# Optimization experiments

Measured on AMD Instinct MI355X. Metric: run time of the kernel, lower is better.

## Reference

```python
import jax, jax.numpy as jnp
import numpy as np

B, N, D = 2, 2048, 1024
H, FD, HD = 16, 16, 64
ENC = 512
EPS = 1e-12
RD = 4.0            # sqrt(scale_dim=feature_dim=16)
RRD = 2.0           # sqrt(RD)
R2 = float(np.sqrt(2.0))


def taylor_exp(x):
    # x: [..., fd] -> [..., 1 + fd + fd*fd]
    x2 = (x[..., :, None] * x[..., None, :]).reshape(*x.shape[:-1], FD * FD) / R2
    return jnp.concatenate([jnp.ones_like(x[..., :1]), x / RRD, x2 / RD], axis=-1)


def setup_inputs() -> dict:
    key = jax.random.key(0)
    ks = jax.random.split(key, 7)
    s = 1.0 / np.sqrt(D)
    x = jax.random.normal(ks[0], (B, N, D), dtype=jnp.float32)
    Wq = jax.random.normal(ks[1], (H * FD, D), dtype=jnp.float32) * s
    Wk = jax.random.normal(ks[2], (H * FD, D), dtype=jnp.float32) * s
    Wv = jax.random.normal(ks[3], (H * HD, D), dtype=jnp.float32) * s
    Wk_enc = jax.random.normal(ks[4], (H * FD, D), dtype=jnp.float32) * s
    Wv_enc = jax.random.normal(ks[5], (H * HD, D), dtype=jnp.float32) * s
    Wout = jax.random.normal(ks[6], (D, H * HD), dtype=jnp.float32) * s
    return {"x": x, "Wq": Wq, "Wk": Wk, "Wv": Wv,
            "Wk_enc": Wk_enc, "Wv_enc": Wv_enc, "Wout": Wout}


def reference(x, Wq, Wk, Wv, Wk_enc, Wv_enc, Wout):
    b, n, _ = x.shape
    # projections -> [b, h, n, *]
    q = (x @ Wq.T).reshape(b, n, H, FD).transpose(0, 2, 1, 3)
    k = (x @ Wk.T).reshape(b, n, H, FD).transpose(0, 2, 1, 3)
    v = (x @ Wv.T).reshape(b, n, H, HD).transpose(0, 2, 1, 3)
    # encoder prefix
    x_enc = x[:, :ENC]
    k_enc = (x_enc @ Wk_enc.T).reshape(b, ENC, H, FD).transpose(0, 2, 1, 3)
    v_enc = (x_enc @ Wv_enc.T).reshape(b, ENC, H, HD).transpose(0, 2, 1, 3)
    # Taylor feature maps: fd -> 1 + fd + fd^2 = 273
    k_enc_f = taylor_exp(k_enc)
    q_f = taylor_exp(q)
    k_f = taylor_exp(k)
    # causal decoder attention (unnormalized)
    A_qk = jnp.einsum('bhnd,bhmd->bhnm', q_f, k_f)
    A_qk = jnp.tril(A_qk)
    y1 = jnp.einsum('bhnm,bhme->bhne', A_qk, v)
    # cross attention to encoder prefix
    A_qk2 = jnp.einsum('bhnd,bhmd->bhnm', q_f, k_enc_f)
    y2 = jnp.einsum('bhnm,bhme->bhne', A_qk2, v_enc)
    # shared normalizer: enc sum + causal cumsum of decoder key features
    k_state = k_enc_f.sum(axis=2, keepdims=True) + jnp.cumsum(k_f, axis=2)
    z = 1.0 / ((q_f * k_state).sum(axis=-1) + EPS)  # [b, h, n]
    out = (y1 + y2) * z[..., None]                  # [b, h, n, hd]
    out = out.transpose(0, 2, 1, 3).reshape(b, n, H * HD)
    return out @ Wout.T
```

## Files before the change

kernel.cpp:

```cpp
#include <hip/hip_runtime.h>

#define B_    2
#define N_    2048
#define H_    16
#define HD_   64
#define ENC_  512
#define FP_   288
#define CHK_  64
#define NC_   32
#define SSZ_  18720
#define C2C_  0.17677669529663687f
#define EPS_  1e-12f

using s8v   = __attribute__((ext_vector_type(8))) short;
using s4v   = __attribute__((ext_vector_type(4))) short;
using h8v   = __attribute__((ext_vector_type(8))) _Float16;
using f4v   = __attribute__((ext_vector_type(4))) float;
using u16x4 = __attribute__((ext_vector_type(4))) unsigned short;
typedef unsigned short ushort_t;

__device__ __forceinline__ unsigned short f16q(float x) {
    _Float16 h = (_Float16)x;
    return __builtin_bit_cast(unsigned short, h);
}
__device__ __forceinline__ float f16f(unsigned short u) {
    return (float)__builtin_bit_cast(_Float16, u);
}
__device__ __forceinline__ u16x4 f16q4(float4 v) {
    return (u16x4){f16q(v.x), f16q(v.y), f16q(v.z), f16q(v.w)};
}

#define MFMAH_ __builtin_amdgcn_mfma_f32_16x16x32_f16

__device__ __forceinline__ void gld16(const void* g, void* l) {
    __builtin_amdgcn_global_load_lds(
        (const __attribute__((address_space(1))) unsigned int*)g,
        (__attribute__((address_space(3))) unsigned int*)l, 16, 0, 0);
}

__device__ __forceinline__ int xcd_swz(int b, int nwg) {
    int q = nwg >> 3, r = nwg & 7;
    int xcd = b & 7, loc = b >> 3;
    return (xcd < r ? xcd * (q + 1) : r * (q + 1) + (xcd - r) * q) + loc;
}

#define X_F4   1048576
#define W1_F4  393216
#define W2_F4  327680
#define WO_F4  262144

__global__ __launch_bounds__(256) void split_all(
    const float* __restrict__ x,
    const float* __restrict__ Wq, const float* __restrict__ Wk,
    const float* __restrict__ Wv, const float* __restrict__ Wke,
    const float* __restrict__ Wve, const float* __restrict__ Wout,
    ushort_t* __restrict__ xh,
    ushort_t* __restrict__ w1, ushort_t* __restrict__ w2,
    ushort_t* __restrict__ wo)
{
    int gid = blockIdx.x * 256 + threadIdx.x;
    if (gid < X_F4) {
        ((u16x4*)xh)[gid] = f16q4(((const float4*)x)[gid]);
    } else if (gid < X_F4 + W1_F4) {
        int i = gid - X_F4;
        int row = i >> 8, c4 = i & 255;
        const float* s = (row < 256) ? Wq + (size_t)row * 1024
                       : (row < 512) ? Wk + (size_t)(row - 256) * 1024
                                     : Wv + (size_t)(row - 512) * 1024;
        ((u16x4*)w1)[i] = f16q4(*(const float4*)(s + c4 * 4));
    } else if (gid < X_F4 + W1_F4 + W2_F4) {
        int i = gid - X_F4 - W1_F4;
        int row = i >> 8, c4 = i & 255;
        const float* s = (row < 256) ? Wke + (size_t)row * 1024
                                     : Wve + (size_t)(row - 256) * 1024;
        ((u16x4*)w2)[i] = f16q4(*(const float4*)(s + c4 * 4));
    } else {
        int i = gid - X_F4 - W1_F4 - W2_F4;
        ((u16x4*)wo)[i] = f16q4(((const float4*)Wout)[i]);
    }
}

template <int SHIFT>
__device__ __forceinline__ void bg128(
    const ushort_t* __restrict__ Ah, const ushort_t* __restrict__ Wh,
    int bx, int by, int rowjump,
    ushort_t* SM, f4v (&acc)[4][4])
{
    int t = threadIdx.x;
    int w = t >> 6, lane = t & 63;
    int row0 = by * 128, col0 = bx * 128;
    int wrow = (w >> 1) * 64, wcol = (w & 1) * 64;
    int fr = lane & 15, g = lane >> 4;

    int c0 = lane, c1 = 64 + lane;
    int r0 = w * 32 + (c0 >> 2), k80 = (c0 & 3) * 8;
    int r1 = w * 32 + (c1 >> 2), k81 = (c1 & 3) * 8;
    int gr0 = row0 + r0, gr1 = row0 + r1;
    size_t a0 = (size_t)(gr0 >> SHIFT) * rowjump + (gr0 & ((1 << SHIFT) - 1));
    size_t a1 = (size_t)(gr1 >> SHIFT) * rowjump + (gr1 & ((1 << SHIFT) - 1));
    const ushort_t* pA0 = Ah + a0 * 1024 + k80;
    const ushort_t* pA1 = Ah + a1 * 1024 + k81;
    const ushort_t* pW0 = Wh + (size_t)(col0 + r0) * 1024 + k80;
    const ushort_t* pW1 = Wh + (size_t)(col0 + r1) * 1024 + k81;
    int woff = w * 1024;

    #pragma unroll
    for (int mt = 0; mt < 4; ++mt)
        #pragma unroll
        for (int nt = 0; nt < 4; ++nt) acc[mt][nt] = (f4v){0.f, 0.f, 0.f, 0.f};

    auto STAGE = [&](int buf, int k0) {
        ushort_t* Bp = SM + buf * 8192;
        gld16(pA0 + k0, Bp + woff);
        gld16(pA1 + k0, Bp + woff + 512);
        gld16(pW0 + k0, Bp + 4096 + woff);
        gld16(pW1 + k0, Bp + 4096 + woff + 512);
    };

    STAGE(0, 0);
    __syncthreads();
    int cur = 0;
    for (int k0 = 0; k0 < 1024; k0 += 32) {
        if (k0 + 32 < 1024) STAGE(cur ^ 1, k0 + 32);
        ushort_t* Bp = SM + cur * 8192;
        h8v a_h[4], b_[4];
        #pragma unroll
        for (int mt = 0; mt < 4; ++mt)
            a_h[mt] = *(const h8v*)&Bp[(wrow + mt * 16 + fr) * 32 + g * 8];
        #pragma unroll
        for (int nt = 0; nt < 4; ++nt)
            b_[nt] = *(const h8v*)&Bp[4096 + (wcol + nt * 16 + fr) * 32 + g * 8];
        #pragma unroll
        for (int mt = 0; mt < 4; ++mt)
            #pragma unroll
            for (int nt = 0; nt < 4; ++nt)
                acc[mt][nt] = MFMAH_(a_h[mt], b_[nt], acc[mt][nt], 0, 0, 0);
        __syncthreads();
        cur ^= 1;
    }
}

__global__ __launch_bounds__(256) void proj2(
    const ushort_t* __restrict__ xh,
    const ushort_t* __restrict__ w1, const ushort_t* __restrict__ w2,
    float* __restrict__ tmpq, float* __restrict__ tmpk, float* __restrict__ v,
    float* __restrict__ tmpke, float* __restrict__ ve)
{
    __shared__ ushort_t SM[16384];
    f4v acc[4][4];
    int blk = xcd_swz(blockIdx.x, 464);
    int t = threadIdx.x, w = t >> 6, lane = t & 63;
    int wrow = (w >> 1) * 64, wcol = (w & 1) * 64;
    int fr = lane & 15, g = lane >> 4;

    if (blk < 384) {
        int bx = blk % 12, by = blk / 12;
        bg128<12>(xh, w1, bx, by, 0, SM, acc);
        int row0 = by * 128, col0 = bx * 128;
        #pragma unroll
        for (int mt = 0; mt < 4; ++mt)
            #pragma unroll
            for (int nt = 0; nt < 4; ++nt)
                #pragma unroll
                for (int r4 = 0; r4 < 4; ++r4) {
                    int r  = row0 + wrow + mt * 16 + g * 4 + r4;
                    int cc = col0 + wcol + nt * 16 + fr;
                    float val = acc[mt][nt][r4];
                    if (cc < 256)      tmpq[(size_t)r * 256 + cc] = val;
                    else if (cc < 512) tmpk[(size_t)r * 256 + (cc - 256)] = val;
                    else {
                        int c2 = cc - 512, hh = c2 >> 6, jj = c2 & 63;
                        int bb = r >> 11, n = r & 2047;
                        v[(((size_t)(bb * 16 + hh)) * 2048 + n) * 64 + jj] = val;
                    }
                }
    } else {
        int r2 = blk - 384;
        int bx = r2 % 10, by = r2 / 10;
        bg128<9>(xh, w2, bx, by, 2048, SM, acc);
        int row0 = by * 128, col0 = bx * 128;
        #pragma unroll
        for (int mt = 0; mt < 4; ++mt)
            #pragma unroll
            for (int nt = 0; nt < 4; ++nt)
                #pragma unroll
                for (int r4 = 0; r4 < 4; ++r4) {
                    int r  = row0 + wrow + mt * 16 + g * 4 + r4;
                    int cc = col0 + wcol + nt * 16 + fr;
                    float val = acc[mt][nt][r4];
                    if (cc < 256) tmpke[(size_t)r * 256 + cc] = val;
                    else {
                        int c2 = cc - 256, hh = c2 >> 6, jj = c2 & 63;
                        int bb = r >> 9, n = r & 511;
                        ve[(((size_t)(bb * 16 + hh)) * 512 + n) * 64 + jj] = val;
                    }
                }
    }
}

__global__ __launch_bounds__(256) void out_gemm(
    const ushort_t* __restrict__ Atn, const ushort_t* __restrict__ Wh,
    float* __restrict__ out)
{
    __shared__ ushort_t SM[16384];
    f4v acc[4][4];
    int blk = xcd_swz(blockIdx.x, 256);
    int bx = blk & 7, by = blk >> 3;
    bg128<12>(Atn, Wh, bx, by, 0, SM, acc);
    int t = threadIdx.x, w = t >> 6, lane = t & 63;
    int wrow = (w >> 1) * 64, wcol = (w & 1) * 64;
    int fr = lane & 15, g = lane >> 4;
    int row0 = by * 128, col0 = bx * 128;
    #pragma unroll
    for (int mt = 0; mt < 4; ++mt)
        #pragma unroll
        for (int nt = 0; nt < 4; ++nt)
            #pragma unroll
            for (int r4 = 0; r4 < 4; ++r4) {
                int r  = row0 + wrow + mt * 16 + g * 4 + r4;
                int cc = col0 + wcol + nt * 16 + fr;
                out[(size_t)r * 1024 + cc] = acc[mt][nt][r4];
            }
}

__device__ __forceinline__ void st_stage(
    const float* __restrict__ Kp, const float* __restrict__ V,
    size_t krow0, size_t vrow0, int h, int t,
    float* ksT, ushort_t* VTH)
{
    {
        int r = t >> 2, q4 = t & 3;
        float4 kv = *(const float4*)&Kp[(krow0 + r) * 256 + h * 16 + q4 * 4];
        ksT[(q4 * 4 + 0) * 68 + r] = kv.x;
        ksT[(q4 * 4 + 1) * 68 + r] = kv.y;
        ksT[(q4 * 4 + 2) * 68 + r] = kv.z;
        ksT[(q4 * 4 + 3) * 68 + r] = kv.w;
    }
    if (t < 64) ksT[16 * 68 + t] = 1.0f;
    {
        int r = t & 63, jg = t >> 6;
        #pragma unroll
        for (int cc = 0; cc < 4; ++cc) {
            float4 vv = *(const float4*)&V[(vrow0 + r) * HD_ + jg * 16 + cc * 4];
            float vals[4] = {vv.x, vv.y, vv.z, vv.w};
            #pragma unroll
            for (int e = 0; e < 4; ++e) {
                int j = jg * 16 + cc * 4 + e;
                VTH[j * 72 + r] = f16q(vals[e]);
            }
        }
    }
    if (t < 64) VTH[64 * 72 + t] = 0x3C00;
}

__device__ __forceinline__ void st_ftile(
    const float* ksT, int ft, int fr, int g,
    const h8v (&AHf)[2][5], f4v (&acc)[5])
{
    int f = ft * 16 + fr;
    int fi, fj; float scale;
    if (f == 0)       { fi = 16; fj = 16; scale = 1.0f; }
    else if (f < 17)  { fi = f - 1; fj = 16; scale = 0.5f; }
    else if (f < 273) { fi = (f - 17) >> 4; fj = (f - 17) & 15; scale = C2C_; }
    else              { fi = 16; fj = 16; scale = 0.0f; }
    #pragma unroll
    for (int ks2 = 0; ks2 < 2; ++ks2) {
        const float* pa = ksT + fi * 68 + ks2 * 32 + g * 8;
        const float* pb = ksT + fj * 68 + ks2 * 32 + g * 8;
        h8v bv;
        #pragma unroll
        for (int e = 0; e < 8; ++e) bv[e] = (_Float16)(pa[e] * pb[e] * scale);
        #pragma unroll
        for (int jt = 0; jt < 5; ++jt)
            acc[jt] = MFMAH_(AHf[ks2][jt], bv, acc[jt], 0, 0, 0);
    }
}

__global__ __launch_bounds__(256) void state_all(
    const float* __restrict__ Kpe, const float* __restrict__ Ve, ushort_t* __restrict__ Se,
    const float* __restrict__ Kpc, const float* __restrict__ Vc, ushort_t* __restrict__ Sc)
{
    __shared__ float ksT[17 * 68];
    __shared__ ushort_t VTH[80 * 72];
    int blk = blockIdx.x, t = threadIdx.x;
    int w = t >> 6, lane = t & 63, fr = lane & 15, g = lane >> 4;

    for (int i = t; i < 15 * 72; i += 256) VTH[65 * 72 + i] = 0;

    if (blk >= 160) {
        int b2 = blk - 160;
        int c = b2 & 31, bh = b2 >> 5;
        int b = bh >> 4, h = bh & 15;
        ushort_t* Sg = Sc + ((size_t)bh * NC_ + c) * SSZ_;
        st_stage(Kpc, Vc, (size_t)b * 2048 + c * 64, (size_t)bh * 2048 + c * 64,
                 h, t, ksT, VTH);
        __syncthreads();
        h8v AHf[2][5];
        #pragma unroll
        for (int ks2 = 0; ks2 < 2; ++ks2)
            #pragma unroll
            for (int jt = 0; jt < 5; ++jt)
                AHf[ks2][jt] = *(const h8v*)&VTH[(jt * 16 + fr) * 72 + ks2 * 32 + g * 8];
        for (int ft = w; ft < 18; ft += 4) {
            f4v acc[5];
            #pragma unroll
            for (int jt = 0; jt < 5; ++jt) acc[jt] = (f4v){0.f, 0.f, 0.f, 0.f};
            st_ftile(ksT, ft, fr, g, AHf, acc);
            #pragma unroll
            for (int jt = 0; jt < 5; ++jt)
                #pragma unroll
                for (int r4 = 0; r4 < 4; ++r4) {
                    int j = jt * 16 + g * 4 + r4;
                    if (j < 65) Sg[(size_t)j * FP_ + ft * 16 + fr] = f16q(acc[jt][r4]);
                }
        }
    } else {
        int bh = blk / 5, fg = blk % 5;
        int b = bh >> 4, h = bh & 15;
        int ft = fg * 4 + w;
        ushort_t* Sg = Se + (size_t)bh * SSZ_;
        f4v acc[5];
        #pragma unroll
        for (int jt = 0; jt < 5; ++jt) acc[jt] = (f4v){0.f, 0.f, 0.f, 0.f};
        for (int m0 = 0; m0 < 512; m0 += 64) {
            if (m0) __syncthreads();
            st_stage(Kpe, Ve, (size_t)b * 512 + m0, (size_t)bh * 512 + m0,
                     h, t, ksT, VTH);
            __syncthreads();
            if (ft < 18) {
                h8v AHf[2][5];
                #pragma unroll
                for (int ks2 = 0; ks2 < 2; ++ks2)
                    #pragma unroll
                    for (int jt = 0; jt < 5; ++jt)
                        AHf[ks2][jt] = *(const h8v*)&VTH[(jt * 16 + fr) * 72 + ks2 * 32 + g * 8];
                st_ftile(ksT, ft, fr, g, AHf, acc);
            }
        }
        if (ft < 18) {
            #pragma unroll
            for (int jt = 0; jt < 5; ++jt)
                #pragma unroll
                for (int r4 = 0; r4 < 4; ++r4) {
                    int j = jt * 16 + g * 4 + r4;
                    if (j < 65) Sg[(size_t)j * FP_ + ft * 16 + fr] = f16q(acc[jt][r4]);
                }
        }
    }
}

__global__ __launch_bounds__(256) void prefix_scan(
    ushort_t* __restrict__ Sloc, const ushort_t* __restrict__ Senc)
{
    const int Q = SSZ_ / 4;
    int gid = blockIdx.x * 256 + threadIdx.x;
    if (gid >= 32 * Q) return;
    int bh = gid / Q, e = gid - bh * Q;
    s4v ev = *(const s4v*)(Senc + (size_t)bh * SSZ_ + e * 4);
    float run[4];
    #pragma unroll
    for (int u = 0; u < 4; ++u) run[u] = f16f((ushort_t)ev[u]);
    ushort_t* Sb = Sloc + (size_t)bh * NC_ * SSZ_ + e * 4;
    #pragma unroll 1
    for (int cb = 0; cb < 8; ++cb) {
        s4v t0 = *(const s4v*)(Sb + (size_t)(cb * 4 + 0) * SSZ_);
        s4v t1 = *(const s4v*)(Sb + (size_t)(cb * 4 + 1) * SSZ_);
        s4v t2 = *(const s4v*)(Sb + (size_t)(cb * 4 + 2) * SSZ_);
        s4v t3 = *(const s4v*)(Sb + (size_t)(cb * 4 + 3) * SSZ_);
        s4v o0, o1, o2, o3;
        #pragma unroll
        for (int u = 0; u < 4; ++u) { o0[u] = (short)f16q(run[u]); run[u] += f16f((ushort_t)t0[u]); }
        #pragma unroll
        for (int u = 0; u < 4; ++u) { o1[u] = (short)f16q(run[u]); run[u] += f16f((ushort_t)t1[u]); }
        #pragma unroll
        for (int u = 0; u < 4; ++u) { o2[u] = (short)f16q(run[u]); run[u] += f16f((ushort_t)t2[u]); }
        #pragma unroll
        for (int u = 0; u < 4; ++u) { o3[u] = (short)f16q(run[u]); run[u] += f16f((ushort_t)t3[u]); }
        *(s4v*)(Sb + (size_t)(cb * 4 + 0) * SSZ_) = o0;
        *(s4v*)(Sb + (size_t)(cb * 4 + 1) * SSZ_) = o1;
        *(s4v*)(Sb + (size_t)(cb * 4 + 2) * SSZ_) = o2;
        *(s4v*)(Sb + (size_t)(cb * 4 + 3) * SSZ_) = o3;
    }
}

template<int FW>
__device__ __forceinline__ void y2_issue(
    const ushort_t* __restrict__ Sth, int f0, int t, s8v& r0, s8v& r1, s8v& r2)
{
    constexpr int NS = FW / 8;
    constexpr int TOT = 65 * NS;
    int s1 = t + 256, s2 = t + 512;
    r0 = *(const s8v*)(Sth + (size_t)(t / NS) * FP_ + f0 + (t % NS) * 8);
    if (s1 < TOT) r1 = *(const s8v*)(Sth + (size_t)(s1 / NS) * FP_ + f0 + (s1 % NS) * 8);
    if (FW == 64 && s2 < TOT) r2 = *(const s8v*)(Sth + (size_t)(s2 / NS) * FP_ + f0 + (s2 % NS) * 8);
}

template<int FW>
__device__ __forceinline__ void y2_write(
    ushort_t* STH, int t, const s8v& r0, const s8v& r1, const s8v& r2)
{
    constexpr int NS = FW / 8;
    constexpr int TOT = 65 * NS;
    int s1 = t + 256, s2 = t + 512;
    *(s8v*)&STH[(t / NS) * 72 + (t % NS) * 8] = r0;
    if (s1 < TOT) *(s8v*)&STH[(s1 / NS) * 72 + (s1 % NS) * 8] = r1;
    if (FW == 64 && s2 < TOT) *(s8v*)&STH[(s2 / NS) * 72 + (s2 % NS) * 8] = r2;
}

template<int FW>
__device__ __forceinline__ void qf_gen(int f0, const float* qs, ushort_t* QF1, int t)
{
    for (int i = t; i < 64 * FW; i += 256) {
        int row = i / FW, cc = i % FW;
        int f = f0 + cc;
        float qv;
        if (f == 0)       qv = 1.0f;
        else if (f < 17)  qv = qs[row * 20 + (f - 1)] * 0.5f;
        else if (f < 273) qv = qs[row * 20 + ((f - 17) >> 4)] * qs[row * 20 + ((f - 17) & 15)] * C2C_;
        else              qv = 0.0f;
        QF1[row * 72 + cc] = f16q(qv);
    }
}

template<int FW>
__device__ __forceinline__ void y2_mfma(
    const ushort_t* QF1, const ushort_t* STH,
    f4v (&acc)[5], int w, int fr, int g)
{
    #pragma unroll
    for (int ks2 = 0; ks2 < FW / 32; ++ks2) {
        h8v a = *(const h8v*)&QF1[(16 * w + fr) * 72 + ks2 * 32 + g * 8];
        #pragma unroll
        for (int jt = 0; jt < 5; ++jt) {
            h8v b = *(const h8v*)&STH[(jt * 16 + fr) * 72 + ks2 * 32 + g * 8];
            acc[jt] = MFMAH_(a, b, acc[jt], 0, 0, 0);
        }
    }
}

__global__ __launch_bounds__(256) void attn_chunk(
    const float* __restrict__ qp, const float* __restrict__ kp,
    const float* __restrict__ v, const ushort_t* __restrict__ Spre,
    ushort_t* __restrict__ atn)
{
    __shared__ ushort_t U[14976];
    __shared__ float qs[64 * 20];
    __shared__ float den_s[64];
    ushort_t* AH  = U;
    ushort_t* QH  = U + 9216;
    ushort_t* KH  = U + 11776;
    ushort_t* VTH = U + 9216;
    ushort_t* QF1 = U;
    ushort_t* STH = U + 9216;

    int bid = blockIdx.x;
    int bh = bid >> 5, c = bid & 31;
    int b = bh >> 4, h = bh & 15;
    int t = threadIdx.x;
    int w = t >> 6, lane = t & 63, fr = lane & 15, g = lane >> 4;
    int rowbase = b * N_ + c * CHK_;
    const ushort_t* Sth = Spre + ((size_t)bh * NC_ + c) * SSZ_;

    int rqk = t >> 2, q4 = t & 3;
    float4 qv = *(const float4*)&qp[(size_t)(rowbase + rqk) * 256 + h * 16 + q4 * 4];
    float4 kv = *(const float4*)&kp[(size_t)(rowbase + rqk) * 256 + h * 16 + q4 * 4];
    s8v rA0 = {}, rA1 = {}, rA2 = {};
    y2_issue<64>(Sth, 0, t, rA0, rA1, rA2);
    int mv = t & 63, jg0 = t >> 6;
    const float* vr = &v[((size_t)bh * N_ + c * CHK_ + mv) * HD_ + jg0 * 16];
    float4 rv0 = *(const float4*)(vr + 0);
    float4 rv1 = *(const float4*)(vr + 4);
    float4 rv2 = *(const float4*)(vr + 8);
    float4 rv3 = *(const float4*)(vr + 12);

    {
        *(u16x4*)&QH[rqk * 40 + q4 * 4] = f16q4(qv);
        *(u16x4*)&KH[rqk * 40 + q4 * 4] = f16q4(kv);
        u16x4 z4 = (u16x4){0, 0, 0, 0};
        *(u16x4*)&QH[rqk * 40 + 16 + q4 * 4] = z4;
        *(u16x4*)&KH[rqk * 40 + 16 + q4 * 4] = z4;
        qs[rqk * 20 + q4 * 4 + 0] = qv.x;
        qs[rqk * 20 + q4 * 4 + 1] = qv.y;
        qs[rqk * 20 + q4 * 4 + 2] = qv.z;
        qs[rqk * 20 + q4 * 4 + 3] = qv.w;
    }
    __syncthreads();

    {
        h8v qh = *(const h8v*)&QH[(16 * w + fr) * 40 + g * 8];
        f4v sacc[4];
        #pragma unroll
        for (int jt = 0; jt < 4; ++jt) sacc[jt] = (f4v){0.f, 0.f, 0.f, 0.f};
        #pragma unroll
        for (int jt = 0; jt < 4; ++jt) {
            h8v kh = *(const h8v*)&KH[(jt * 16 + fr) * 40 + g * 8];
            sacc[jt] = MFMAH_(qh, kh, sacc[jt], 0, 0, 0);
        }
        __syncthreads();
        #pragma unroll
        for (int jt = 0; jt < 4; ++jt)
            #pragma unroll
            for (int r4 = 0; r4 < 4; ++r4) {
                int row = 16 * w + g * 4 + r4, col = jt * 16 + fr;
                float s = sacc[jt][r4];
                float a = (row >= col) ? (fmaf(s, 0.25f, 1.0f) + s * s * 0.03125f) : 0.f;
                AH[row * 72 + col] = f16q(a);
            }
    }
    {
        int j0 = jg0 * 16;
        VTH[(j0 +  0) * 72 + mv] = f16q(rv0.x); VTH[(j0 +  1) * 72 + mv] = f16q(rv0.y);
        VTH[(j0 +  2) * 72 + mv] = f16q(rv0.z); VTH[(j0 +  3) * 72 + mv] = f16q(rv0.w);
        VTH[(j0 +  4) * 72 + mv] = f16q(rv1.x); VTH[(j0 +  5) * 72 + mv] = f16q(rv1.y);
        VTH[(j0 +  6) * 72 + mv] = f16q(rv1.z); VTH[(j0 +  7) * 72 + mv] = f16q(rv1.w);
        VTH[(j0 +  8) * 72 + mv] = f16q(rv2.x); VTH[(j0 +  9) * 72 + mv] = f16q(rv2.y);
        VTH[(j0 + 10) * 72 + mv] = f16q(rv2.z); VTH[(j0 + 11) * 72 + mv] = f16q(rv2.w);
        VTH[(j0 + 12) * 72 + mv] = f16q(rv3.x); VTH[(j0 + 13) * 72 + mv] = f16q(rv3.y);
        VTH[(j0 + 14) * 72 + mv] = f16q(rv3.z); VTH[(j0 + 15) * 72 + mv] = f16q(rv3.w);
    }
    if (t < 64) VTH[64 * 72 + t] = 0x3C00;
    for (int i = t; i < 15 * 72; i += 256) VTH[65 * 72 + i] = 0;
    __syncthreads();

    f4v acc[5];
    #pragma unroll
    for (int jt = 0; jt < 5; ++jt) acc[jt] = (f4v){0.f, 0.f, 0.f, 0.f};
    #pragma unroll
    for (int ks2 = 0; ks2 < 2; ++ks2) {
        h8v ah = *(const h8v*)&AH[(16 * w + fr) * 72 + ks2 * 32 + g * 8];
        #pragma unroll
        for (int jt = 0; jt < 5; ++jt) {
            h8v b = *(const h8v*)&VTH[(jt * 16 + fr) * 72 + ks2 * 32 + g * 8];
            acc[jt] = MFMAH_(ah, b, acc[jt], 0, 0, 0);
        }
    }
    __syncthreads();

    #pragma unroll
    for (int p = 0; p < 4; ++p) {
        y2_write<64>(STH, t, rA0, rA1, rA2);
        if (p < 3) y2_issue<64>(Sth, (p + 1) * 64, t, rA0, rA1, rA2);
        else       y2_issue<32>(Sth, 256,          t, rA0, rA1, rA2);
        qf_gen<64>(p * 64, qs, QF1, t);
        __syncthreads();
        y2_mfma<64>(QF1, STH, acc, w, fr, g);
        __syncthreads();
    }
    y2_write<32>(STH, t, rA0, rA1, rA2);
    qf_gen<32>(256, qs, QF1, t);
    __syncthreads();
    y2_mfma<32>(QF1, STH, acc, w, fr, g);

    if (fr == 0) {
        #pragma unroll
        for (int r4 = 0; r4 < 4; ++r4)
            den_s[16 * w + g * 4 + r4] = acc[4][r4];
    }
    __syncthreads();
    #pragma unroll
    for (int r4 = 0; r4 < 4; ++r4) {
        float z = 1.0f / (den_s[16 * w + g * 4 + r4] + EPS_);
        int row = rowbase + 16 * w + g * 4 + r4;
        #pragma unroll
        for (int jt = 0; jt < 4; ++jt) {
            float val = acc[jt][r4] * z;
            atn[(size_t)row * 1024 + h * 64 + jt * 16 + fr] = f16q(val);
        }
    }
}

extern "C" void kernel_launch(void* const* d_in, const int* in_sizes, int n_in,
                              void* d_out, int out_size, void* d_ws, size_t ws_size,
                              hipStream_t stream)
{
    const float* x    = (const float*)d_in[0];
    const float* Wq   = (const float*)d_in[1];
    const float* Wk   = (const float*)d_in[2];
    const float* Wv   = (const float*)d_in[3];
    const float* Wke  = (const float*)d_in[4];
    const float* Wve  = (const float*)d_in[5];
    const float* Wout = (const float*)d_in[6];
    float* out = (float*)d_out;
    float* ws  = (float*)d_ws;

    float* tmpq  = ws;
    float* tmpk  = tmpq  + (size_t)1048576;
    float* tmpke = tmpk  + (size_t)1048576;
    float* v     = tmpke + (size_t)262144;
    float* ve    = v     + (size_t)4194304;
    ushort_t* Sloc = (ushort_t*)(ve + 1048576);
    ushort_t* Senc = Sloc + (size_t)19169280;
    ushort_t* xh   = Senc + (size_t)599040;
    ushort_t* wo   = xh   + (size_t)4194304;
    ushort_t* w1 = Sloc;
    ushort_t* w2 = w1 + (size_t)1572864;
    ushort_t* atn = xh;

    dim3 blk(256);

    split_all<<<7936, blk, 0, stream>>>(x, Wq, Wk, Wv, Wke, Wve, Wout,
                                        xh, w1, w2, wo);
    proj2<<<464, blk, 0, stream>>>(xh, w1, w2, tmpq, tmpk, v, tmpke, ve);
    state_all<<<160 + 32 * NC_, blk, 0, stream>>>(tmpke, ve, Senc, tmpk, v, Sloc);
    prefix_scan<<<585, blk, 0, stream>>>(Sloc, Senc);
    attn_chunk<<<32 * NC_, blk, 0, stream>>>(tmpq, tmpk, v, Sloc, atn);
    out_gemm<<<256, blk, 0, stream>>>(atn, wo, out);
}
```

Measured before the change: 109.9 us.

## Store projected q/k/v intermediates as fp16 and fully unroll prefix scan loads

The projection kernel now writes q, k, v and the encoder k/v to the workspace as fp16 instead of fp32. The state and attention kernels read fp16 directly, skipping their own conversion, and use narrower vector loads. This halves the global traffic for these intermediates. Separately, the prefix scan now loads all 32 chunk states into registers before the sequential accumulation, which exposes more memory parallelism at the cost of more registers. Rounding q and k to fp16 before forming the squared Taylor features may lose some accuracy.

```diff
diff --git a/kernel.cpp b/kernel.cpp
--- a/kernel.cpp
+++ b/kernel.cpp
@@ -143,8 +143,8 @@
 __global__ __launch_bounds__(256) void proj2(
     const ushort_t* __restrict__ xh,
     const ushort_t* __restrict__ w1, const ushort_t* __restrict__ w2,
-    float* __restrict__ tmpq, float* __restrict__ tmpk, float* __restrict__ v,
-    float* __restrict__ tmpke, float* __restrict__ ve)
+    ushort_t* __restrict__ tmpq, ushort_t* __restrict__ tmpk, ushort_t* __restrict__ v,
+    ushort_t* __restrict__ tmpke, ushort_t* __restrict__ ve)
 {
     __shared__ ushort_t SM[16384];
     f4v acc[4][4];
@@ -165,7 +165,7 @@
                 for (int r4 = 0; r4 < 4; ++r4) {
                     int r  = row0 + wrow + mt * 16 + g * 4 + r4;
                     int cc = col0 + wcol + nt * 16 + fr;
-                    float val = acc[mt][nt][r4];
+                    ushort_t val = f16q(acc[mt][nt][r4]);
                     if (cc < 256)      tmpq[(size_t)r * 256 + cc] = val;
                     else if (cc < 512) tmpk[(size_t)r * 256 + (cc - 256)] = val;
                     else {
@@ -187,7 +187,7 @@
                 for (int r4 = 0; r4 < 4; ++r4) {
                     int r  = row0 + wrow + mt * 16 + g * 4 + r4;
                     int cc = col0 + wcol + nt * 16 + fr;
-                    float val = acc[mt][nt][r4];
+                    ushort_t val = f16q(acc[mt][nt][r4]);
                     if (cc < 256) tmpke[(size_t)r * 256 + cc] = val;
                     else {
                         int c2 = cc - 256, hh = c2 >> 6, jj = c2 & 63;
@@ -224,31 +224,29 @@
 }
 
 __device__ __forceinline__ void st_stage(
-    const float* __restrict__ Kp, const float* __restrict__ V,
+    const ushort_t* __restrict__ Kp, const ushort_t* __restrict__ V,
     size_t krow0, size_t vrow0, int h, int t,
     float* ksT, ushort_t* VTH)
 {
     {
         int r = t >> 2, q4 = t & 3;
-        float4 kv = *(const float4*)&Kp[(krow0 + r) * 256 + h * 16 + q4 * 4];
-        ksT[(q4 * 4 + 0) * 68 + r] = kv.x;
-        ksT[(q4 * 4 + 1) * 68 + r] = kv.y;
-        ksT[(q4 * 4 + 2) * 68 + r] = kv.z;
-        ksT[(q4 * 4 + 3) * 68 + r] = kv.w;
+        s4v kv = *(const s4v*)&Kp[(krow0 + r) * 256 + h * 16 + q4 * 4];
+        ksT[(q4 * 4 + 0) * 68 + r] = f16f((ushort_t)kv[0]);
+        ksT[(q4 * 4 + 1) * 68 + r] = f16f((ushort_t)kv[1]);
+        ksT[(q4 * 4 + 2) * 68 + r] = f16f((ushort_t)kv[2]);
+        ksT[(q4 * 4 + 3) * 68 + r] = f16f((ushort_t)kv[3]);
     }
     if (t < 64) ksT[16 * 68 + t] = 1.0f;
     {
         int r = t & 63, jg = t >> 6;
-        #pragma unroll
-        for (int cc = 0; cc < 4; ++cc) {
-            float4 vv = *(const float4*)&V[(vrow0 + r) * HD_ + jg * 16 + cc * 4];
-            float vals[4] = {vv.x, vv.y, vv.z, vv.w};
-            #pragma unroll
-            for (int e = 0; e < 4; ++e) {
-                int j = jg * 16 + cc * 4 + e;
-                VTH[j * 72 + r] = f16q(vals[e]);
-            }
-        }
+        const ushort_t* vrow = &V[(vrow0 + r) * HD_ + jg * 16];
+        s8v v0 = *(const s8v*)(vrow);
+        s8v v1 = *(const s8v*)(vrow + 8);
+        int j0 = jg * 16;
+        #pragma unroll
+        for (int e = 0; e < 8; ++e) VTH[(j0 + e) * 72 + r] = (ushort_t)v0[e];
+        #pragma unroll
+        for (int e = 0; e < 8; ++e) VTH[(j0 + 8 + e) * 72 + r] = (ushort_t)v1[e];
     }
     if (t < 64) VTH[64 * 72 + t] = 0x3C00;
 }
@@ -277,8 +275,8 @@
 }
 
 __global__ __launch_bounds__(256) void state_all(
-    const float* __restrict__ Kpe, const float* __restrict__ Ve, ushort_t* __restrict__ Se,
-    const float* __restrict__ Kpc, const float* __restrict__ Vc, ushort_t* __restrict__ Sc)
+    const ushort_t* __restrict__ Kpe, const ushort_t* __restrict__ Ve, ushort_t* __restrict__ Se,
+    const ushort_t* __restrict__ Kpc, const ushort_t* __restrict__ Vc, ushort_t* __restrict__ Sc)
 {
     __shared__ float ksT[17 * 68];
     __shared__ ushort_t VTH[80 * 72];
@@ -361,25 +359,19 @@
     #pragma unroll
     for (int u = 0; u < 4; ++u) run[u] = f16f((ushort_t)ev[u]);
     ushort_t* Sb = Sloc + (size_t)bh * NC_ * SSZ_ + e * 4;
-    #pragma unroll 1
-    for (int cb = 0; cb < 8; ++cb) {
-        s4v t0 = *(const s4v*)(Sb + (size_t)(cb * 4 + 0) * SSZ_);
-        s4v t1 = *(const s4v*)(Sb + (size_t)(cb * 4 + 1) * SSZ_);
-        s4v t2 = *(const s4v*)(Sb + (size_t)(cb * 4 + 2) * SSZ_);
-        s4v t3 = *(const s4v*)(Sb + (size_t)(cb * 4 + 3) * SSZ_);
-        s4v o0, o1, o2, o3;
-        #pragma unroll
-        for (int u = 0; u < 4; ++u) { o0[u] = (short)f16q(run[u]); run[u] += f16f((ushort_t)t0[u]); }
-        #pragma unroll
-        for (int u = 0; u < 4; ++u) { o1[u] = (short)f16q(run[u]); run[u] += f16f((ushort_t)t1[u]); }
-        #pragma unroll
-        for (int u = 0; u < 4; ++u) { o2[u] = (short)f16q(run[u]); run[u] += f16f((ushort_t)t2[u]); }
-        #pragma unroll
-        for (int u = 0; u < 4; ++u) { o3[u] = (short)f16q(run[u]); run[u] += f16f((ushort_t)t3[u]); }
-        *(s4v*)(Sb + (size_t)(cb * 4 + 0) * SSZ_) = o0;
-        *(s4v*)(Sb + (size_t)(cb * 4 + 1) * SSZ_) = o1;
-        *(s4v*)(Sb + (size_t)(cb * 4 + 2) * SSZ_) = o2;
-        *(s4v*)(Sb + (size_t)(cb * 4 + 3) * SSZ_) = o3;
+    s4v tv[NC_];
+    #pragma unroll
+    for (int c2 = 0; c2 < NC_; ++c2)
+        tv[c2] = *(const s4v*)(Sb + (size_t)c2 * SSZ_);
+    #pragma unroll
+    for (int c2 = 0; c2 < NC_; ++c2) {
+        s4v o;
+        #pragma unroll
+        for (int u = 0; u < 4; ++u) {
+            o[u] = (short)f16q(run[u]);
+            run[u] += f16f((ushort_t)tv[c2][u]);
+        }
+        *(s4v*)(Sb + (size_t)c2 * SSZ_) = o;
     }
 }
 
@@ -439,8 +431,8 @@
 }
 
 __global__ __launch_bounds__(256) void attn_chunk(
-    const float* __restrict__ qp, const float* __restrict__ kp,
-    const float* __restrict__ v, const ushort_t* __restrict__ Spre,
+    const ushort_t* __restrict__ qp, const ushort_t* __restrict__ kp,
+    const ushort_t* __restrict__ v, const ushort_t* __restrict__ Spre,
     ushort_t* __restrict__ atn)
 {
     __shared__ ushort_t U[14976];
@@ -462,27 +454,25 @@
     const ushort_t* Sth = Spre + ((size_t)bh * NC_ + c) * SSZ_;
 
     int rqk = t >> 2, q4 = t & 3;
-    float4 qv = *(const float4*)&qp[(size_t)(rowbase + rqk) * 256 + h * 16 + q4 * 4];
-    float4 kv = *(const float4*)&kp[(size_t)(rowbase + rqk) * 256 + h * 16 + q4 * 4];
+    s4v qv = *(const s4v*)&qp[(size_t)(rowbase + rqk) * 256 + h * 16 + q4 * 4];
+    s4v kv = *(const s4v*)&kp[(size_t)(rowbase + rqk) * 256 + h * 16 + q4 * 4];
     s8v rA0 = {}, rA1 = {}, rA2 = {};
     y2_issue<64>(Sth, 0, t, rA0, rA1, rA2);
     int mv = t & 63, jg0 = t >> 6;
-    const float* vr = &v[((size_t)bh * N_ + c * CHK_ + mv) * HD_ + jg0 * 16];
-    float4 rv0 = *(const float4*)(vr + 0);
-    float4 rv1 = *(const float4*)(vr + 4);
-    float4 rv2 = *(const float4*)(vr + 8);
-    float4 rv3 = *(const float4*)(vr + 12);
+    const ushort_t* vr = &v[((size_t)bh * N_ + c * CHK_ + mv) * HD_ + jg0 * 16];
+    s8v rv0 = *(const s8v*)(vr);
+    s8v rv1 = *(const s8v*)(vr + 8);
 
     {
-        *(u16x4*)&QH[rqk * 40 + q4 * 4] = f16q4(qv);
-        *(u16x4*)&KH[rqk * 40 + q4 * 4] = f16q4(kv);
-        u16x4 z4 = (u16x4){0, 0, 0, 0};
-        *(u16x4*)&QH[rqk * 40 + 16 + q4 * 4] = z4;
-        *(u16x4*)&KH[rqk * 40 + 16 + q4 * 4] = z4;
-        qs[rqk * 20 + q4 * 4 + 0] = qv.x;
-        qs[rqk * 20 + q4 * 4 + 1] = qv.y;
-        qs[rqk * 20 + q4 * 4 + 2] = qv.z;
-        qs[rqk * 20 + q4 * 4 + 3] = qv.w;
+        *(s4v*)&QH[rqk * 40 + q4 * 4] = qv;
+        *(s4v*)&KH[rqk * 40 + q4 * 4] = kv;
+        s4v z4 = (s4v){0, 0, 0, 0};
+        *(s4v*)&QH[rqk * 40 + 16 + q4 * 4] = z4;
+        *(s4v*)&KH[rqk * 40 + 16 + q4 * 4] = z4;
+        qs[rqk * 20 + q4 * 4 + 0] = f16f((ushort_t)qv[0]);
+        qs[rqk * 20 + q4 * 4 + 1] = f16f((ushort_t)qv[1]);
+        qs[rqk * 20 + q4 * 4 + 2] = f16f((ushort_t)qv[2]);
+        qs[rqk * 20 + q4 * 4 + 3] = f16f((ushort_t)qv[3]);
     }
     __syncthreads();
 
@@ -509,14 +499,10 @@
     }
     {
         int j0 = jg0 * 16;
-        VTH[(j0 +  0) * 72 + mv] = f16q(rv0.x); VTH[(j0 +  1) * 72 + mv] = f16q(rv0.y);
-        VTH[(j0 +  2) * 72 + mv] = f16q(rv0.z); VTH[(j0 +  3) * 72 + mv] = f16q(rv0.w);
-        VTH[(j0 +  4) * 72 + mv] = f16q(rv1.x); VTH[(j0 +  5) * 72 + mv] = f16q(rv1.y);
-        VTH[(j0 +  6) * 72 + mv] = f16q(rv1.z); VTH[(j0 +  7) * 72 + mv] = f16q(rv1.w);
-        VTH[(j0 +  8) * 72 + mv] = f16q(rv2.x); VTH[(j0 +  9) * 72 + mv] = f16q(rv2.y);
-        VTH[(j0 + 10) * 72 + mv] = f16q(rv2.z); VTH[(j0 + 11) * 72 + mv] = f16q(rv2.w);
-        VTH[(j0 + 12) * 72 + mv] = f16q(rv3.x); VTH[(j0 + 13) * 72 + mv] = f16q(rv3.y);
-        VTH[(j0 + 14) * 72 + mv] = f16q(rv3.z); VTH[(j0 + 15) * 72 + mv] = f16q(rv3.w);
+        #pragma unroll
+        for (int e = 0; e < 8; ++e) VTH[(j0 + e) * 72 + mv] = (ushort_t)rv0[e];
+        #pragma unroll
+        for (int e = 0; e < 8; ++e) VTH[(j0 + 8 + e) * 72 + mv] = (ushort_t)rv1[e];
     }
     if (t < 64) VTH[64 * 72 + t] = 0x3C00;
     for (int i = t; i < 15 * 72; i += 256) VTH[65 * 72 + i] = 0;
@@ -581,17 +567,17 @@
     const float* Wve  = (const float*)d_in[5];
     const float* Wout = (const float*)d_in[6];
     float* out = (float*)d_out;
-    float* ws  = (float*)d_ws;
-
-    float* tmpq  = ws;
-    float* tmpk  = tmpq  + (size_t)1048576;
-    float* tmpke = tmpk  + (size_t)1048576;
-    float* v     = tmpke + (size_t)262144;
-    float* ve    = v     + (size_t)4194304;
-    ushort_t* Sloc = (ushort_t*)(ve + 1048576);
-    ushort_t* Senc = Sloc + (size_t)19169280;
-    ushort_t* xh   = Senc + (size_t)599040;
-    ushort_t* wo   = xh   + (size_t)4194304;
+
+    ushort_t* usws  = (ushort_t*)d_ws;
+    ushort_t* tmpq  = usws;
+    ushort_t* tmpk  = tmpq  + (size_t)1048576;
+    ushort_t* tmpke = tmpk  + (size_t)1048576;
+    ushort_t* v     = tmpke + (size_t)262144;
+    ushort_t* ve    = v     + (size_t)4194304;
+    ushort_t* Sloc  = ve    + (size_t)1048576;
+    ushort_t* Senc  = Sloc  + (size_t)19169280;
+    ushort_t* xh    = Senc  + (size_t)599040;
+    ushort_t* wo    = xh    + (size_t)4194304;
     ushort_t* w1 = Sloc;
     ushort_t* w2 = w1 + (size_t)1572864;
     ushort_t* atn = xh;
```

Result: faster. 103.5 us (median of 3 runs) (-5.8%).
